# Optimization experiments

Hardware: AMD Instinct MI355X
Metric: run time of the kernel (lower is better)

The kernel has to match this reference:

```python
import jax, jax.numpy as jnp
import numpy as np

EMBED = 1024
HEADS = 16
HEAD_DIM = EMBED // HEADS


def setup_inputs() -> dict:
    key = jax.random.key(0)
    ks = jax.random.split(key, 8)
    N, S, E = 4, 2048, EMBED
    inp = {
        "queries": jax.random.normal(ks[0], (N, S, E), dtype=jnp.float32),
        "keys": jax.random.normal(ks[1], (N, S, E), dtype=jnp.float32),
        "values": jax.random.normal(ks[2], (N, S, E), dtype=jnp.float32),
        # projection weights, stored as (in, out) so y = x @ W
        "Wq": jax.random.normal(ks[3], (E, E), dtype=jnp.float32) / np.sqrt(E),
        "Wk": jax.random.normal(ks[4], (E, E), dtype=jnp.float32) / np.sqrt(E),
        "Wv": jax.random.normal(ks[5], (E, E), dtype=jnp.float32) / np.sqrt(E),
        "Wo": jax.random.normal(ks[6], (E, E), dtype=jnp.float32) / np.sqrt(E),
        "bo": jax.random.normal(ks[7], (E,), dtype=jnp.float32) * 0.01,
    }
    return inp


def reference(queries, keys, values, Wq, Wk, Wv, Wo, bo):
    N, Sq, E = queries.shape
    Sk = keys.shape[1]
    H, D = HEADS, HEAD_DIM
    # linear projections (no bias)
    q = (queries @ Wq).reshape(N, Sq, H, D)
    k = (keys @ Wk).reshape(N, Sk, H, D)
    v = (values @ Wv).reshape(N, Sk, H, D)
    # energy: [N, H, Sq, Sk]
    energy = jnp.einsum("nqhd,nkhd->nhqk", q, k)
    attn = jax.nn.softmax(energy / np.sqrt(D).astype(np.float32), axis=3)
    # out: [N, Sq, H, D] -> [N, Sq, E]
    out = jnp.einsum("nhqk,nkhd->nqhd", attn, v).reshape(N, Sq, E)
    return out @ Wo + bo
```

## Files before the change

### kernel.cpp

```cpp
#include <hip/hip_runtime.h>
#include <hip/hip_bf16.h>

typedef __bf16 bf16;
typedef bf16 bf16x4v __attribute__((ext_vector_type(4)));
typedef bf16 bf16x8 __attribute__((ext_vector_type(8)));
typedef float f32x4 __attribute__((ext_vector_type(4)));
typedef float f32x16 __attribute__((ext_vector_type(16)));
typedef unsigned int uint;
typedef unsigned short ushort;

static constexpr int E   = 1024;
static constexpr int SEQ = 2048;
static constexpr int NB  = 4;
static constexpr int M   = NB * SEQ;

__device__ __forceinline__ void async16(const void* g, void* l) {
  __builtin_amdgcn_global_load_lds(
      (const __attribute__((address_space(1))) void*)g,
      (__attribute__((address_space(3))) void*)l, 16, 0, 0);
}

__device__ __forceinline__ uint pack2(float a, float b) {
  bf16 x = (bf16)a, y = (bf16)b;
  return (uint)__builtin_bit_cast(ushort, x) |
         ((uint)__builtin_bit_cast(ushort, y) << 16);
}

__global__ __launch_bounds__(256) void k_conv3(const float* __restrict__ s0,
                                               const float* __restrict__ s1,
                                               const float* __restrict__ s2,
                                               bf16* __restrict__ d0,
                                               bf16* __restrict__ d1,
                                               bf16* __restrict__ d2) {
  const float* src = blockIdx.z == 0 ? s0 : blockIdx.z == 1 ? s1 : s2;
  bf16* dst        = blockIdx.z == 0 ? d0 : blockIdx.z == 1 ? d1 : d2;
  size_t i = (size_t)blockIdx.x * 256 + threadIdx.x;
  const float4* s = reinterpret_cast<const float4*>(src) + i * 2;
  float4 a = s[0], b = s[1];
  bf16x8 o;
  o[0] = (bf16)a.x; o[1] = (bf16)a.y; o[2] = (bf16)a.z; o[3] = (bf16)a.w;
  o[4] = (bf16)b.x; o[5] = (bf16)b.y; o[6] = (bf16)b.z; o[7] = (bf16)b.w;
  *reinterpret_cast<bf16x8*>(dst + i * 8) = o;
}

__global__ __launch_bounds__(256) void k_convW(const float* s0, const float* s1,
                                               const float* s2, const float* s3,
                                               bf16* d0, bf16* d1, bf16* d2, bf16* d3) {
  __shared__ float tile[64][65];
  const float* W = blockIdx.z == 0 ? s0 : blockIdx.z == 1 ? s1 : blockIdx.z == 2 ? s2 : s3;
  bf16* WT       = blockIdx.z == 0 ? d0 : blockIdx.z == 1 ? d1 : blockIdx.z == 2 ? d2 : d3;
  const int tx = threadIdx.x & 63, ty = threadIdx.x >> 6;
  const int nb = blockIdx.x * 64, kb = blockIdx.y * 64;
#pragma unroll
  for (int r = 0; r < 16; ++r)
    tile[ty + r * 4][tx] = W[(size_t)(kb + ty + r * 4) * E + nb + tx];
  __syncthreads();
#pragma unroll
  for (int r = 0; r < 16; ++r)
    WT[(size_t)(nb + ty + r * 4) * E + kb + tx] = (bf16)tile[tx][ty + r * 4];
}

template <int MODE>
__global__ __launch_bounds__(256) void k_gemm(const bf16* __restrict__ A,
                                              const bf16* __restrict__ BT,
                                              void* __restrict__ Cout,
                                              const float* __restrict__ bias) {
  __shared__ __align__(16) bf16 As[2][128 * 32];
  __shared__ __align__(16) bf16 Bs[2][128 * 32];
  const int t = threadIdx.x;
  const int l = t & 63, w = t >> 6;
  const int lo = l & 15, hi = l >> 4;
  const int wm = w >> 1, wn = w & 1;
  const int m0 = blockIdx.x * 128, n0 = blockIdx.y * 128;
  f32x4 acc[4][4] = {};

  const int r0 = t >> 2, s0 = t & 3;
  const bf16* ga0 = A + (size_t)(m0 + r0) * E + s0 * 8;
  const bf16* ga1 = ga0 + (size_t)64 * E;
  const bf16* gb0 = BT + (size_t)(n0 + r0) * E + s0 * 8;
  const bf16* gb1 = gb0 + (size_t)64 * E;

  auto stage = [&](int buf, int kk) {
    char* la = (char*)As[buf] + t * 16;
    char* lb = (char*)Bs[buf] + t * 16;
    async16(ga0 + kk, la);
    async16(ga1 + kk, la + 4096);
    async16(gb0 + kk, lb);
    async16(gb1 + kk, lb + 4096);
  };

  stage(0, 0);
  __syncthreads();
  int cur = 0;
  for (int kk = 0; kk < E; kk += 32) {
    if (kk + 32 < E) stage(cur ^ 1, kk + 32);
    const bf16* AsC = As[cur];
    const bf16* BsC = Bs[cur];
    bf16x8 af[4], bfr[4];
#pragma unroll
    for (int mi = 0; mi < 4; ++mi)
      af[mi] = *(const bf16x8*)&AsC[(wm * 64 + mi * 16 + lo) * 32 + hi * 8];
#pragma unroll
    for (int ni = 0; ni < 4; ++ni)
      bfr[ni] = *(const bf16x8*)&BsC[(wn * 64 + ni * 16 + lo) * 32 + hi * 8];
    __builtin_amdgcn_s_setprio(1);
#pragma unroll
    for (int mi = 0; mi < 4; ++mi)
#pragma unroll
      for (int ni = 0; ni < 4; ++ni)
        acc[mi][ni] = __builtin_amdgcn_mfma_f32_16x16x32_bf16(af[mi], bfr[ni],
                                                              acc[mi][ni], 0, 0, 0);
    __builtin_amdgcn_s_setprio(0);
    __syncthreads();
    cur ^= 1;
  }

  const int mrow = m0 + wm * 64, ncol = n0 + wn * 64;
  if (MODE == 2) {
    float* C = (float*)Cout;
    float bv[4];
#pragma unroll
    for (int ni = 0; ni < 4; ++ni) bv[ni] = bias[ncol + ni * 16 + lo];
#pragma unroll
    for (int mi = 0; mi < 4; ++mi)
#pragma unroll
      for (int ni = 0; ni < 4; ++ni)
#pragma unroll
        for (int i = 0; i < 4; ++i)
          C[(size_t)(mrow + mi * 16 + hi * 4 + i) * E + ncol + ni * 16 + lo] =
              acc[mi][ni][i] + bv[ni];
  } else if (MODE == 1) {
    bf16* VtO = (bf16*)Cout;
#pragma unroll
    for (int mi = 0; mi < 4; ++mi) {
      int mrow_ = mrow + mi * 16 + hi * 4;
      int nb_ = mrow_ >> 11, sidx = mrow_ & 2047;
#pragma unroll
      for (int ni = 0; ni < 4; ++ni) {
        int col = ncol + ni * 16 + lo;
        bf16x4v v4;
#pragma unroll
        for (int j = 0; j < 4; ++j) v4[j] = (bf16)acc[mi][ni][j];
        *(bf16x4v*)(VtO + ((size_t)(nb_ * 16 + (col >> 6)) * 64 + (col & 63)) * SEQ + sidx) = v4;
      }
    }
  } else {
    constexpr float sc = (MODE == 3) ? 0.18033688011112042f : 1.0f;
    bf16* C = (bf16*)Cout;
#pragma unroll
    for (int mi = 0; mi < 4; ++mi)
#pragma unroll
      for (int ni = 0; ni < 4; ++ni)
#pragma unroll
        for (int i = 0; i < 4; ++i)
          C[(size_t)(mrow + mi * 16 + hi * 4 + i) * E + ncol + ni * 16 + lo] =
              (bf16)(acc[mi][ni][i] * sc);
  }
}

__global__ __launch_bounds__(256, 2) void k_attn(const bf16* __restrict__ Qp,
                                                 const bf16* __restrict__ Kp,
                                                 const bf16* __restrict__ Vt,
                                                 bf16* __restrict__ Z) {
  __shared__ __align__(16) bf16 KV[2][2][64 * 64];
  const int t = threadIdx.x, l = t & 63, w = t >> 6;
  const int qq = l & 31, hi = l >> 5, l7 = l & 7;
  const int p = blockIdx.x;
  const int lswz = (p & 7) * 64 + (p >> 3);
  const int qb = lswz & 7, nh = lswz >> 3;
  const int n = nh >> 4, h = nh & 15;
  const int q0w = qb * 256 + w * 64;
  const int krow = (qq & 0x13) | ((qq & 4) << 1) | ((qq & 8) >> 1);

  bf16x8 qf[2][4];
#pragma unroll
  for (int j = 0; j < 2; ++j) {
    const bf16* qrow = Qp + (size_t)(n * SEQ + q0w + j * 32 + qq) * E + h * 64;
#pragma unroll
    for (int ks = 0; ks < 4; ++ks) qf[j][ks] = *(const bf16x8*)(qrow + ks * 16 + hi * 8);
  }

  const bf16* kbase = Kp + (size_t)n * SEQ * E + h * 64;
  const bf16* vbase = Vt + (size_t)nh * 64 * SEQ;
  const int r_st = t >> 3, s_st = t & 7;
  const int gs = (s_st ^ (r_st & 7)) * 8;

  auto stage = [&](int buf, int kt) {
    char* lk = (char*)KV[buf][0] + t * 16;
    char* lv = (char*)KV[buf][1] + t * 16;
    async16(kbase + (size_t)(kt + r_st) * E + gs, lk);
    async16(kbase + (size_t)(kt + r_st + 32) * E + gs, lk + 4096);
    async16(vbase + (size_t)r_st * SEQ + kt + gs, lv);
    async16(vbase + (size_t)(r_st + 32) * SEQ + kt + gs, lv + 4096);
  };

  f32x16 oacc[2][2] = {};
  float l_r[2] = {0.f, 0.f};

  stage(0, 0);
  __syncthreads();
  int cur = 0;
  for (int kt = 0; kt < SEQ; kt += 64) {
    if (kt + 64 < SEQ) stage(cur ^ 1, kt + 64);
    const bf16* KsC = KV[cur][0];
    const bf16* VsC = KV[cur][1];

    f32x16 sacc[2][2];
    __builtin_amdgcn_s_setprio(1);
#pragma unroll
    for (int kb = 0; kb < 2; ++kb) {
      bf16x8 kfr[4];
#pragma unroll
      for (int ks = 0; ks < 4; ++ks)
        kfr[ks] = *(const bf16x8*)(KsC + (kb * 32 + krow) * 64 + (((ks * 2 + hi) ^ (krow & 7)) * 8));
#pragma unroll
      for (int j = 0; j < 2; ++j) {
        f32x16 a = {};
#pragma unroll
        for (int ks = 0; ks < 4; ++ks)
          a = __builtin_amdgcn_mfma_f32_32x32x16_bf16(kfr[ks], qf[j][ks], a, 0, 0, 0);
        sacc[j][kb] = a;
      }
    }
    __builtin_amdgcn_s_setprio(0);

    uint wv[2][2][8];
#pragma unroll
    for (int j = 0; j < 2; ++j) {
      float rs = 0.f;
#pragma unroll
      for (int kb = 0; kb < 2; ++kb) {
        float pv[16];
#pragma unroll
        for (int r = 0; r < 16; ++r) {
          float e = __builtin_amdgcn_exp2f(sacc[j][kb][r]);
          pv[r] = e;
          rs += e;
        }
#pragma unroll
        for (int i = 0; i < 8; ++i) wv[j][kb][i] = pack2(pv[2 * i], pv[2 * i + 1]);
      }
      l_r[j] += rs;
    }

    __builtin_amdgcn_s_setprio(1);
#pragma unroll
    for (int d = 0; d < 2; ++d)
#pragma unroll
      for (int kb = 0; kb < 2; ++kb)
#pragma unroll
        for (int ks2 = 0; ks2 < 2; ++ks2) {
          const int ks = kb * 2 + ks2;
          bf16x8 vf = *(const bf16x8*)(VsC + (d * 32 + qq) * 64 + (((ks * 2 + hi) ^ l7) * 8));
#pragma unroll
          for (int j = 0; j < 2; ++j) {
            bf16x8 pf;
            uint* pp = (uint*)&pf;
            pp[0] = wv[j][kb][ks2 * 4 + 0];
            pp[1] = wv[j][kb][ks2 * 4 + 1];
            pp[2] = wv[j][kb][ks2 * 4 + 2];
            pp[3] = wv[j][kb][ks2 * 4 + 3];
            oacc[j][d] = __builtin_amdgcn_mfma_f32_32x32x16_bf16(vf, pf, oacc[j][d], 0, 0, 0);
          }
        }
    __builtin_amdgcn_s_setprio(0);
    __syncthreads();
    cur ^= 1;
  }

#pragma unroll
  for (int j = 0; j < 2; ++j) {
    const float lt = l_r[j] + __shfl_xor(l_r[j], 32);
    const float inv = 1.f / lt;
    bf16* zrow = Z + (size_t)(n * SEQ + q0w + j * 32 + qq) * E + h * 64;
#pragma unroll
    for (int d = 0; d < 2; ++d)
#pragma unroll
      for (int g = 0; g < 4; ++g) {
        bf16x4v v4;
#pragma unroll
        for (int jj = 0; jj < 4; ++jj) v4[jj] = (bf16)(oacc[j][d][g * 4 + jj] * inv);
        *(bf16x4v*)(zrow + d * 32 + g * 8 + hi * 4) = v4;
      }
  }
}

extern "C" void kernel_launch(void* const* d_in, const int* in_sizes, int n_in,
                              void* d_out, int out_size, void* d_ws, size_t ws_size,
                              hipStream_t stream) {
  const float* q_in = (const float*)d_in[0];
  const float* k_in = (const float*)d_in[1];
  const float* v_in = (const float*)d_in[2];
  const float* Wq   = (const float*)d_in[3];
  const float* Wk   = (const float*)d_in[4];
  const float* Wv   = (const float*)d_in[5];
  const float* Wo   = (const float*)d_in[6];
  const float* bo   = (const float*)d_in[7];

  char* ws = (char*)d_ws;
  const size_t SZ = (size_t)M * E * 2;
  bf16* qc   = (bf16*)(ws);
  bf16* kc   = (bf16*)(ws + SZ);
  bf16* vc   = (bf16*)(ws + 2 * SZ);
  bf16* qp   = (bf16*)(ws + 3 * SZ);
  bf16* kp   = (bf16*)(ws + 4 * SZ);
  bf16* vt   = (bf16*)(ws + 5 * SZ);
  bf16* zz   = (bf16*)(ws + 6 * SZ);
  bf16* wT   = (bf16*)(ws + 7 * SZ);
  bf16* wqT = wT;
  bf16* wkT = wT + (size_t)E * E;
  bf16* wvT = wT + 2 * (size_t)E * E;
  bf16* woT = wT + 3 * (size_t)E * E;

  dim3 b256(256);
  k_convW<<<dim3(16, 16, 4), b256, 0, stream>>>(Wq, Wk, Wv, Wo, wqT, wkT, wvT, woT);
  k_conv3<<<dim3(4096, 1, 3), b256, 0, stream>>>(q_in, k_in, v_in, qc, kc, vc);

  k_gemm<3><<<dim3(64, 8), b256, 0, stream>>>(qc, wqT, qp, nullptr);
  k_gemm<0><<<dim3(64, 8), b256, 0, stream>>>(kc, wkT, kp, nullptr);
  k_gemm<1><<<dim3(64, 8), b256, 0, stream>>>(vc, wvT, vt, nullptr);

  k_attn<<<dim3(512), b256, 0, stream>>>(qp, kp, vt, zz);
  k_gemm<2><<<dim3(64, 8), b256, 0, stream>>>(zz, woT, d_out, bo);
}
```

Before: 212.9 us.

## Load attention K/V fragments directly from global memory, drop LDS staging

The attention kernel no longer stages K and V tiles into double-buffered shared memory with async loads. Each wave now reads its K and V MFMA fragments straight from global memory (relying on L2/cache), which removes the block barriers. Blocks shrink to 128 threads (2 waves, 128 queries each) and the grid doubles to 1024 blocks. The trade-off is more global/L2 traffic, since K/V reuse across waves is lost, and exposed load latency without explicit prefetch.

```diff
diff --git a/kernel.cpp b/kernel.cpp
--- a/kernel.cpp
+++ b/kernel.cpp
@@ -158,18 +158,17 @@
   }
 }
 
-__global__ __launch_bounds__(256, 2) void k_attn(const bf16* __restrict__ Qp,
+__global__ __launch_bounds__(128, 2) void k_attn(const bf16* __restrict__ Qp,
                                                  const bf16* __restrict__ Kp,
                                                  const bf16* __restrict__ Vt,
                                                  bf16* __restrict__ Z) {
-  __shared__ __align__(16) bf16 KV[2][2][64 * 64];
   const int t = threadIdx.x, l = t & 63, w = t >> 6;
-  const int qq = l & 31, hi = l >> 5, l7 = l & 7;
+  const int qq = l & 31, hi = l >> 5;
   const int p = blockIdx.x;
-  const int lswz = (p & 7) * 64 + (p >> 3);
-  const int qb = lswz & 7, nh = lswz >> 3;
+  const int lswz = (p & 7) * 128 + (p >> 3);
+  const int qb = lswz & 15, nh = lswz >> 4;
   const int n = nh >> 4, h = nh & 15;
-  const int q0w = qb * 256 + w * 64;
+  const int q0w = qb * 128 + w * 64;
   const int krow = (qq & 0x13) | ((qq & 4) << 1) | ((qq & 8) >> 1);
 
   bf16x8 qf[2][4];
@@ -180,65 +179,59 @@
     for (int ks = 0; ks < 4; ++ks) qf[j][ks] = *(const bf16x8*)(qrow + ks * 16 + hi * 8);
   }
 
-  const bf16* kbase = Kp + (size_t)n * SEQ * E + h * 64;
-  const bf16* vbase = Vt + (size_t)nh * 64 * SEQ;
-  const int r_st = t >> 3, s_st = t & 7;
-  const int gs = (s_st ^ (r_st & 7)) * 8;
-
-  auto stage = [&](int buf, int kt) {
-    char* lk = (char*)KV[buf][0] + t * 16;
-    char* lv = (char*)KV[buf][1] + t * 16;
-    async16(kbase + (size_t)(kt + r_st) * E + gs, lk);
-    async16(kbase + (size_t)(kt + r_st + 32) * E + gs, lk + 4096);
-    async16(vbase + (size_t)r_st * SEQ + kt + gs, lv);
-    async16(vbase + (size_t)(r_st + 32) * SEQ + kt + gs, lv + 4096);
-  };
+  const bf16* kptr = Kp + ((size_t)n * SEQ + krow) * E + h * 64 + hi * 8;
+  const bf16* vptr = Vt + ((size_t)nh * 64 + qq) * SEQ + hi * 8;
 
   f32x16 oacc[2][2] = {};
   float l_r[2] = {0.f, 0.f};
 
-  stage(0, 0);
-  __syncthreads();
-  int cur = 0;
   for (int kt = 0; kt < SEQ; kt += 64) {
-    if (kt + 64 < SEQ) stage(cur ^ 1, kt + 64);
-    const bf16* KsC = KV[cur][0];
-    const bf16* VsC = KV[cur][1];
+    const bf16* kp0 = kptr + (size_t)kt * E;
+    const bf16* vp0 = vptr + kt;
+
+    bf16x8 kfr[2][4];
+#pragma unroll
+    for (int kb2 = 0; kb2 < 2; ++kb2)
+#pragma unroll
+      for (int ks = 0; ks < 4; ++ks)
+        kfr[kb2][ks] = *(const bf16x8*)(kp0 + (size_t)kb2 * 32 * E + ks * 16);
 
     f32x16 sacc[2][2];
     __builtin_amdgcn_s_setprio(1);
 #pragma unroll
-    for (int kb = 0; kb < 2; ++kb) {
-      bf16x8 kfr[4];
-#pragma unroll
-      for (int ks = 0; ks < 4; ++ks)
-        kfr[ks] = *(const bf16x8*)(KsC + (kb * 32 + krow) * 64 + (((ks * 2 + hi) ^ (krow & 7)) * 8));
+    for (int kb2 = 0; kb2 < 2; ++kb2)
 #pragma unroll
       for (int j = 0; j < 2; ++j) {
         f32x16 a = {};
 #pragma unroll
         for (int ks = 0; ks < 4; ++ks)
-          a = __builtin_amdgcn_mfma_f32_32x32x16_bf16(kfr[ks], qf[j][ks], a, 0, 0, 0);
-        sacc[j][kb] = a;
-      }
-    }
+          a = __builtin_amdgcn_mfma_f32_32x32x16_bf16(kfr[kb2][ks], qf[j][ks], a, 0, 0, 0);
+        sacc[j][kb2] = a;
+      }
     __builtin_amdgcn_s_setprio(0);
+
+    bf16x8 vfr[2][4];
+#pragma unroll
+    for (int d = 0; d < 2; ++d)
+#pragma unroll
+      for (int ks = 0; ks < 4; ++ks)
+        vfr[d][ks] = *(const bf16x8*)(vp0 + (size_t)d * 32 * SEQ + ks * 16);
 
     uint wv[2][2][8];
 #pragma unroll
     for (int j = 0; j < 2; ++j) {
       float rs = 0.f;
 #pragma unroll
-      for (int kb = 0; kb < 2; ++kb) {
+      for (int kb2 = 0; kb2 < 2; ++kb2) {
         float pv[16];
 #pragma unroll
         for (int r = 0; r < 16; ++r) {
-          float e = __builtin_amdgcn_exp2f(sacc[j][kb][r]);
+          float e = __builtin_amdgcn_exp2f(sacc[j][kb2][r]);
           pv[r] = e;
           rs += e;
         }
 #pragma unroll
-        for (int i = 0; i < 8; ++i) wv[j][kb][i] = pack2(pv[2 * i], pv[2 * i + 1]);
+        for (int i = 0; i < 8; ++i) wv[j][kb2][i] = pack2(pv[2 * i], pv[2 * i + 1]);
       }
       l_r[j] += rs;
     }
@@ -247,25 +240,19 @@
 #pragma unroll
     for (int d = 0; d < 2; ++d)
 #pragma unroll
-      for (int kb = 0; kb < 2; ++kb)
-#pragma unroll
-        for (int ks2 = 0; ks2 < 2; ++ks2) {
-          const int ks = kb * 2 + ks2;
-          bf16x8 vf = *(const bf16x8*)(VsC + (d * 32 + qq) * 64 + (((ks * 2 + hi) ^ l7) * 8));
-#pragma unroll
-          for (int j = 0; j < 2; ++j) {
-            bf16x8 pf;
-            uint* pp = (uint*)&pf;
-            pp[0] = wv[j][kb][ks2 * 4 + 0];
-            pp[1] = wv[j][kb][ks2 * 4 + 1];
-            pp[2] = wv[j][kb][ks2 * 4 + 2];
-            pp[3] = wv[j][kb][ks2 * 4 + 3];
-            oacc[j][d] = __builtin_amdgcn_mfma_f32_32x32x16_bf16(vf, pf, oacc[j][d], 0, 0, 0);
-          }
+      for (int ks = 0; ks < 4; ++ks) {
+#pragma unroll
+        for (int j = 0; j < 2; ++j) {
+          bf16x8 pf;
+          uint* pp = (uint*)&pf;
+          pp[0] = wv[j][ks >> 1][(ks & 1) * 4 + 0];
+          pp[1] = wv[j][ks >> 1][(ks & 1) * 4 + 1];
+          pp[2] = wv[j][ks >> 1][(ks & 1) * 4 + 2];
+          pp[3] = wv[j][ks >> 1][(ks & 1) * 4 + 3];
+          oacc[j][d] = __builtin_amdgcn_mfma_f32_32x32x16_bf16(vfr[d][ks], pf, oacc[j][d], 0, 0, 0);
         }
+      }
     __builtin_amdgcn_s_setprio(0);
-    __syncthreads();
-    cur ^= 1;
   }
 
 #pragma unroll
@@ -320,6 +307,6 @@
   k_gemm<0><<<dim3(64, 8), b256, 0, stream>>>(kc, wkT, kp, nullptr);
   k_gemm<1><<<dim3(64, 8), b256, 0, stream>>>(vc, wvT, vt, nullptr);
 
-  k_attn<<<dim3(512), b256, 0, stream>>>(qp, kp, vt, zz);
+  k_attn<<<dim3(1024), dim3(128), 0, stream>>>(qp, kp, vt, zz);
   k_gemm<2><<<dim3(64, 8), b256, 0, stream>>>(zz, woT, d_out, bo);
 }
```

New measurement: 255.2 us. +19.8%, slower.
